# Performance work log

Hardware: AMD Instinct MI355X
Metric: run time of the kernel (lower is better)

The kernel has to match this reference:

```python
import jax, jax.numpy as jnp
import numpy as np

GRID_SIZE = 8
MARGIN = 1.0
NUM_NEG = 4
SOS_NEG = 8
LOSS_LAMBDA = 1.0
IMG_H, IMG_W = 960, 1280  # desc2 is the stride-GRID_SIZE feature map of this image
BIG = 5.0    # fill for radius-masked entries in FOS distance matrix (> max unit-desc dist 2)
HUGE = 1e6   # fill for invalid entries in SOS candidate scores


def _l2n(x, eps=1e-8):
    return x / (jnp.linalg.norm(x, axis=-1, keepdims=True) + eps)


def _pdist(a, b, eps=1e-12):
    # a: B x N x C, b: B x M x C -> B x N x M euclidean distances
    sq = (jnp.sum(a * a, -1)[..., :, None] + jnp.sum(b * b, -1)[..., None, :]
          - 2.0 * jnp.einsum('bnc,bmc->bnm', a, b))
    return jnp.sqrt(jnp.maximum(sq, eps))


def _bilinear(desc, pts):
    # desc: B x C x H x W, pts: B x N x 2 in (y, x) image-pixel coords -> B x N x C
    B, C, H, W = desc.shape
    g = pts / GRID_SIZE - 0.5  # image coords -> feature-grid coords
    gy = jnp.clip(g[..., 0], 0.0, H - 1.0)
    gx = jnp.clip(g[..., 1], 0.0, W - 1.0)
    y0 = jnp.clip(jnp.floor(gy).astype(jnp.int32), 0, H - 2)
    x0 = jnp.clip(jnp.floor(gx).astype(jnp.int32), 0, W - 2)
    wy = (gy - y0)[:, None, :]
    wx = (gx - x0)[:, None, :]
    flat = desc.reshape(B, C, H * W)
    gat = lambda yi, xi: jnp.take_along_axis(flat, (yi * W + xi)[:, None, :], axis=2)
    v00, v01 = gat(y0, x0), gat(y0, x0 + 1)
    v10, v11 = gat(y0 + 1, x0), gat(y0 + 1, x0 + 1)
    out = (v00 * (1 - wy) * (1 - wx) + v01 * (1 - wy) * wx
           + v10 * wy * (1 - wx) + v11 * wy * wx)
    return out.transpose(0, 2, 1)


def _forward(kp1, w_kp1, kp1_desc, desc2, homo12):
    r = 2.0 * GRID_SIZE  # spatial masking radius
    d1 = _l2n(kp1_desc)                       # B x N x C
    w_desc = _l2n(_bilinear(desc2, w_kp1))    # B x N x C interpolated warped descriptors

    # visibility of kp1 under homography homo12 (kp stored as (y, x))
    ones = jnp.ones_like(kp1[..., :1])
    p = jnp.concatenate([kp1[..., 1:2], kp1[..., 0:1], ones], -1)  # (x, y, 1)
    q = jnp.einsum('bij,bnj->bni', homo12, p)
    qx = q[..., 0] / (q[..., 2] + 1e-8)
    qy = q[..., 1] / (q[..., 2] + 1e-8)
    vis = ((qx >= 0) & (qx < IMG_W) & (qy >= 0) & (qy < IMG_H)).astype(d1.dtype)
    denom = jnp.sum(vis) + 1e-8

    # ---- FOS: hard quad triplet with radius masking ----
    pos = jnp.sqrt(jnp.sum((d1 - w_desc) ** 2, -1) + 1e-12)  # B x N
    D = _pdist(d1, w_desc)          # B x N x N cross descriptor distances
    s22 = _pdist(w_kp1, w_kp1)      # B x N x N warped-coordinate distances
    Dm = jnp.where(s22 <= r, BIG, D)  # mask spatial near-positives (incl. diagonal)
    neg1 = -jax.lax.top_k(-Dm, NUM_NEG)[0]                       # hardest negs per row anchor
    neg2 = -jax.lax.top_k(-Dm.transpose(0, 2, 1), NUM_NEG)[0]    # per column anchor
    t1 = jnp.mean(jax.nn.relu(MARGIN + pos[..., None] - neg1), -1)
    t2 = jnp.mean(jax.nn.relu(MARGIN + pos[..., None] - neg2), -1)
    fos = jnp.sum(vis * 0.5 * (t1 + t2)) / denom

    # ---- SOS: radius-masked second-order similarity regularizer ----
    s11 = _pdist(kp1, kp1)
    d11 = _pdist(d1, d1)
    d22 = _pdist(w_desc, w_desc)
    valid = (s11 > r) & (s22 > r)
    score = jnp.where(valid, d11, HUGE)
    nscore, idx = jax.lax.top_k(-score, SOS_NEG)  # sos_neg hardest valid neighbors
    sel_d11 = -nscore
    sel_d22 = jnp.take_along_axis(d22, idx, axis=2)
    diff2 = jnp.where(sel_d11 < HUGE * 0.1, (sel_d11 - sel_d22) ** 2, 0.0)
    sos_i = jnp.sqrt(jnp.sum(diff2, -1) + 1e-12)
    sos = jnp.sum(vis * sos_i) / denom

    return (fos + sos) * LOSS_LAMBDA


def setup_inputs() -> dict:
    key = jax.random.key(0)
    k1, k2, k3, k4, k5 = jax.random.split(key, 5)
    B, N, C, H, W = 2, 4096, 128, 120, 160
    scale = jnp.array([IMG_H - 1.0, IMG_W - 1.0], dtype=jnp.float32)
    kp1 = jax.random.uniform(k1, (B, N, 2), dtype=jnp.float32) * scale
    w_kp1 = jax.random.uniform(k2, (B, N, 2), dtype=jnp.float32) * scale
    kp1_desc = jax.random.normal(k3, (B, N, C), dtype=jnp.float32)
    desc2 = jax.random.normal(k4, (B, C, H, W), dtype=jnp.float32)
    homo12 = (jnp.tile(jnp.eye(3, dtype=jnp.float32), (B, 1, 1))
              + 0.001 * jax.random.normal(k5, (B, 3, 3), dtype=jnp.float32))
    return {'kp1': kp1, 'w_kp1': w_kp1, 'kp1_desc': kp1_desc,
            'desc2': desc2, 'homo12': homo12}


def reference(kp1, w_kp1, kp1_desc, desc2, homo12):
    return _forward(kp1, w_kp1, kp1_desc, desc2, homo12)
```

## Files before the change

kernel.cpp:

```cpp
#include <hip/hip_runtime.h>
#include <hip/hip_fp16.h>
#include <math.h>

#define NPTS 4096
#define CDIM 128
#define FH 120
#define FW 160
#define PIX (FH * FW)

typedef __attribute__((ext_vector_type(8))) short short8_t;
typedef __attribute__((ext_vector_type(4))) float float4_t;
typedef __attribute__((ext_vector_type(2))) unsigned short ushort2_t;

#define OFF_FRAG  0
#define OFF_WDB   1048576
#define OFF_JA    1572864
#define OFF_JB    1605632
#define OFF_POS   1622016
#define OFF_VIS   1630208
#define OFF_ACC   1638400
#define OFF_PARTS 1638416
#define OFF_D2T   2031632
#define OFF_END   4489232

__device__ __forceinline__ unsigned short f2bf(float f) {
  unsigned int u = __float_as_uint(f);
  u = (u + 0x7fffu + ((u >> 16) & 1u)) >> 16;
  return (unsigned short)u;
}

__device__ __forceinline__ float wavesum(float v) {
#pragma unroll
  for (int off = 1; off < 64; off <<= 1) v += __shfl_xor(v, off, 64);
  return v;
}

__global__ __launch_bounds__(256) void transpose_desc2(
    const float* __restrict__ d2, unsigned short* __restrict__ out) {
  __shared__ unsigned short tile[64][130];
  const int bp = blockIdx.x;
  const int b = bp / 300;
  const int p0 = (bp - b * 300) * 64;
  const int tid = threadIdx.x;
  const int grp = tid >> 6, lp = tid & 63;
#pragma unroll 4
  for (int r = 0; r < 32; ++r) {
    int c = (r << 2) | grp;
    float v = d2[((size_t)b * CDIM + c) * PIX + p0 + lp];
    tile[lp][c] = __half_as_ushort(__float2half(v));
  }
  __syncthreads();
  unsigned int* ob = (unsigned int*)(out + ((size_t)b * PIX + p0) * CDIM);
#pragma unroll
  for (int i = 0; i < 16; ++i) {
    int u = (i << 8) | tid;
    int p = u >> 6, cc = (u & 63) << 1;
    unsigned int lo = tile[p][cc], hi = tile[p][cc + 1];
    ob[u] = lo | (hi << 16);
  }
}

#define PREP_TAIL() do {                                                        \
  {                                                                             \
    const int T = (p & (NPTS - 1)) >> 4, cRow = p & 15;                         \
    const int kcL = lane >> 4, quadL = (lane >> 2) & 3, jjL = (lane & 3) * 2;   \
    const size_t off = (size_t)(quadL * 16 + cRow) * 8 + jjL;                   \
    const size_t tb = (((size_t)b * 256 + T) * 2) * 4;                          \
    ushort2_t st; st.x = f2bf(d0); st.y = f2bf(d1v);                            \
    ushort2_t sw; sw.x = f2bf(e0); sw.y = f2bf(e1);                             \
    *(ushort2_t*)(frag + (tb + kcL) * 512 + off) = st;                          \
    *(ushort2_t*)(frag + (tb + 4 + kcL) * 512 + off) = sw;                      \
    ushort2_t swr; swr.x = f2bf(e0); swr.y = f2bf(e1);                          \
    *(ushort2_t*)(wdb + (size_t)p * CDIM + c2) = swr;                           \
  }                                                                             \
  float dd0 = d0 - e0, dd1 = d1v - e1;                                          \
  float ssp = wavesum(dd0 * dd0 + dd1 * dd1);                                   \
  if (lane == 0) {                                                              \
    pos[p] = sqrtf(ssp + 1e-12f);                                               \
    float ky = kp1[p * 2 + 0], kx = kp1[p * 2 + 1];                             \
    jA[p] = make_float4(ky, kx, y, x);                                          \
    jB[p] = make_float2(n1, n2);                                                \
    const float* h = homo + b * 9;                                              \
    float t0 = h[0] * kx + h[1] * ky + h[2];                                    \
    float t1 = h[3] * kx + h[4] * ky + h[5];                                    \
    float t2 = h[6] * kx + h[7] * ky + h[8];                                    \
    float qx = t0 / (t2 + 1e-8f), qy = t1 / (t2 + 1e-8f);                       \
    vis[p] = (qx >= 0.0f && qx < 1280.0f && qy >= 0.0f && qy < 960.0f)          \
                 ? 1.0f : 0.0f;                                                 \
  }                                                                             \
} while (0)

__global__ __launch_bounds__(256) void prep_t(
    const float* __restrict__ kp1, const float* __restrict__ wkp1,
    const float* __restrict__ desc, const unsigned short* __restrict__ d2t,
    const float* __restrict__ homo,
    unsigned short* __restrict__ frag, unsigned short* __restrict__ wdb,
    float4* __restrict__ jA, float2* __restrict__ jB,
    float* __restrict__ pos, float* __restrict__ vis, float* __restrict__ acc) {
  const int tid = threadIdx.x;
  if (blockIdx.x == 0 && tid < 4) acc[tid] = 0.0f;
  const int p = blockIdx.x * 4 + (tid >> 6);
  const int lane = tid & 63;
  const int b = p >> 12;
  const int c2 = lane * 2;

  float2 v = *(const float2*)(desc + (size_t)p * CDIM + c2);
  float ss = wavesum(v.x * v.x + v.y * v.y);
  float inv = 1.0f / (sqrtf(ss) + 1e-8f);
  float d0 = v.x * inv, d1v = v.y * inv;
  float n1 = ss * inv * inv;

  float y = wkp1[p * 2 + 0], x = wkp1[p * 2 + 1];
  float gy = fminf(fmaxf(y * 0.125f - 0.5f, 0.0f), (float)(FH - 1));
  float gx = fminf(fmaxf(x * 0.125f - 0.5f, 0.0f), (float)(FW - 1));
  int y0 = (int)floorf(gy); y0 = min(max(y0, 0), FH - 2);
  int x0 = (int)floorf(gx); x0 = min(max(x0, 0), FW - 2);
  float wy = gy - (float)y0, wx = gx - (float)x0;
  float w00 = (1 - wy) * (1 - wx), w01 = (1 - wy) * wx;
  float w10 = wy * (1 - wx), w11 = wy * wx;
  const unsigned int* t00 = (const unsigned int*)
      (d2t + ((size_t)b * PIX + y0 * FW + x0) * CDIM) + lane;
  unsigned int u00 = t00[0], u01 = t00[64];
  unsigned int u10 = t00[FW * 64], u11 = t00[FW * 64 + 64];
  float2 f00 = __half22float2(*(const __half2*)&u00);
  float2 f01 = __half22float2(*(const __half2*)&u01);
  float2 f10 = __half22float2(*(const __half2*)&u10);
  float2 f11 = __half22float2(*(const __half2*)&u11);
  float wv0 = f00.x * w00 + f01.x * w01 + f10.x * w10 + f11.x * w11;
  float wv1 = f00.y * w00 + f01.y * w01 + f10.y * w10 + f11.y * w11;
  float ss2 = wavesum(wv0 * wv0 + wv1 * wv1);
  float inv2 = 1.0f / (sqrtf(ss2) + 1e-8f);
  float e0 = wv0 * inv2, e1 = wv1 * inv2;
  float n2 = ss2 * inv2 * inv2;

  PREP_TAIL();
}

__global__ __launch_bounds__(256) void prep_g(
    const float* __restrict__ kp1, const float* __restrict__ wkp1,
    const float* __restrict__ desc, const float* __restrict__ desc2,
    const float* __restrict__ homo,
    unsigned short* __restrict__ frag, unsigned short* __restrict__ wdb,
    float4* __restrict__ jA, float2* __restrict__ jB,
    float* __restrict__ pos, float* __restrict__ vis, float* __restrict__ acc) {
  const int tid = threadIdx.x;
  if (blockIdx.x == 0 && tid < 4) acc[tid] = 0.0f;
  const int p = blockIdx.x * 4 + (tid >> 6);
  const int lane = tid & 63;
  const int b = p >> 12;
  const int c2 = lane * 2;

  float2 v = *(const float2*)(desc + (size_t)p * CDIM + c2);
  float ss = wavesum(v.x * v.x + v.y * v.y);
  float inv = 1.0f / (sqrtf(ss) + 1e-8f);
  float d0 = v.x * inv, d1v = v.y * inv;
  float n1 = ss * inv * inv;

  float y = wkp1[p * 2 + 0], x = wkp1[p * 2 + 1];
  float gy = fminf(fmaxf(y * 0.125f - 0.5f, 0.0f), (float)(FH - 1));
  float gx = fminf(fmaxf(x * 0.125f - 0.5f, 0.0f), (float)(FW - 1));
  int y0 = (int)floorf(gy); y0 = min(max(y0, 0), FH - 2);
  int x0 = (int)floorf(gx); x0 = min(max(x0, 0), FW - 2);
  float wy = gy - (float)y0, wx = gx - (float)x0;
  float w00 = (1 - wy) * (1 - wx), w01 = (1 - wy) * wx;
  float w10 = wy * (1 - wx), w11 = wy * wx;
  const float* q0 = desc2 + ((size_t)b * CDIM + c2) * PIX + y0 * FW + x0;
  const float* q1 = q0 + PIX;
  float wv0 = q0[0] * w00 + q0[1] * w01 + q0[FW] * w10 + q0[FW + 1] * w11;
  float wv1 = q1[0] * w00 + q1[1] * w01 + q1[FW] * w10 + q1[FW + 1] * w11;
  float ss2 = wavesum(wv0 * wv0 + wv1 * wv1);
  float inv2 = 1.0f / (sqrtf(ss2) + 1e-8f);
  float e0 = wv0 * inv2, e1 = wv1 * inv2;
  float n2 = ss2 * inv2 * inv2;

  PREP_TAIL();
}

__device__ __forceinline__ void ins4m(float v, float* L) {
  float p0 = L[0]; L[0] = fmaxf(L[0], v);
  float p1 = L[1]; L[1] = __builtin_amdgcn_fmed3f(p0, L[1], v);
  float p2 = L[2]; L[2] = __builtin_amdgcn_fmed3f(p1, L[2], v);
  L[3] = __builtin_amdgcn_fmed3f(p2, L[3], v);
}
__device__ __forceinline__ void ins6m(float v, float* L) {
  float p0 = L[0]; L[0] = fmaxf(L[0], v);
  float p1 = L[1]; L[1] = __builtin_amdgcn_fmed3f(p0, L[1], v);
  float p2 = L[2]; L[2] = __builtin_amdgcn_fmed3f(p1, L[2], v);
  float p3 = L[3]; L[3] = __builtin_amdgcn_fmed3f(p2, L[3], v);
  float p4 = L[4]; L[4] = __builtin_amdgcn_fmed3f(p3, L[4], v);
  L[5] = __builtin_amdgcn_fmed3f(p4, L[5], v);
}
__device__ __forceinline__ void ins10m(float v, float* L) {
  float p0 = L[0]; L[0] = fmaxf(L[0], v);
  float pk = p0;
#pragma unroll
  for (int k = 1; k < 9; ++k) {
    float cur = L[k];
    L[k] = __builtin_amdgcn_fmed3f(pk, cur, v);
    pk = cur;
  }
  L[9] = __builtin_amdgcn_fmed3f(pk, L[9], v);
}

__device__ __forceinline__ float packkey(float s, int j) {
  return __uint_as_float((__float_as_uint(s) & 0xFFFFF000u) | (unsigned)j);
}

#define TILE_COMPUTE(AD, AW, NA, NB, J0) do {                                   \
  float4_t aD = {0,0,0,0}, aDt = {0,0,0,0}, a11 = {0,0,0,0};                    \
  _Pragma("unroll")                                                             \
  for (int kc = 0; kc < 4; ++kc) {                                              \
    aD  = __builtin_amdgcn_mfma_f32_16x16x32_bf16(AW[kc], Bd[kc], aD,  0,0,0);  \
    aDt = __builtin_amdgcn_mfma_f32_16x16x32_bf16(AD[kc], Bw[kc], aDt, 0,0,0);  \
    a11 = __builtin_amdgcn_mfma_f32_16x16x32_bf16(AD[kc], Bd[kc], a11, 0,0,0);  \
  }                                                                             \
  const float nj1[4] = {NA.x, NA.z, NB.x, NB.z};                                \
  const float nj2[4] = {NA.y, NA.w, NB.y, NB.w};                                \
  _Pragma("unroll")                                                             \
  for (int reg = 0; reg < 4; ++reg) {                                           \
    const int jj = (J0) + (quad << 2) + reg;                                    \
    ins4m(packkey(fmaf(2.0f, aD[reg],  -nj2[reg]), jj), fD);                    \
    ins4m(packkey(fmaf(2.0f, aDt[reg], -nj1[reg]), jj), fDt);                   \
    ins6m(packkey(fmaf(2.0f, a11[reg], -nj1[reg]), jj), fS);                    \
  }                                                                             \
} while (0)

__global__ __launch_bounds__(256, 3) void loss_main(
    const unsigned short* __restrict__ frag,
    const float2* __restrict__ jBg, float* __restrict__ parts) {
  __shared__ float mb[4][16][24];

  const int tid = threadIdx.x;
  const int bid = blockIdx.x;
  const int b = bid & 1;
  const int half = (bid >> 1) & 1;
  const int g = bid >> 2;
  const int i0 = g * 16;
  const int wave = tid >> 6, lane = tid & 63;
  const int c = lane & 15, quad = lane >> 4;
  const int base = b * NPTS;

  short8_t Bd[4], Bw[4];
  {
    const unsigned short* fb = frag + ((((size_t)b * 256 + g) * 2) * 4) * 512 + (size_t)lane * 8;
#pragma unroll
    for (int kc = 0; kc < 4; ++kc) {
      Bd[kc] = *(const short8_t*)(fb + kc * 512);
      Bw[kc] = *(const short8_t*)(fb + (4 + kc) * 512);
    }
  }

  float fD[4], fDt[4], fS[6];
#pragma unroll
  for (int k = 0; k < 4; ++k) { fD[k] = -1e30f; fDt[k] = -1e30f; }
#pragma unroll
  for (int k = 0; k < 6; ++k) fS[k] = -1e30f;

  const int jstart = (half << 11) | (wave << 9);
  const unsigned short* fa = frag + (((size_t)b * 256 + (jstart >> 4)) * 8) * 512 + (size_t)lane * 8;
  const float2* jbb = jBg + base;

  short8_t A0d[4], A0w[4], A1d[4], A1w[4];
#pragma unroll
  for (int kc = 0; kc < 4; ++kc) {
    A0d[kc] = *(const short8_t*)(fa + kc * 512);
    A0w[kc] = *(const short8_t*)(fa + (4 + kc) * 512);
  }
  float4 n0a = *(const float4*)(jbb + jstart + (quad << 2));
  float4 n0b = *(const float4*)(jbb + jstart + (quad << 2) + 2);
  float4 n1a, n1b;

  for (int t = 0; t < 32; t += 2) {
    const unsigned short* f1 = fa + 4096;
#pragma unroll
    for (int kc = 0; kc < 4; ++kc) {
      A1d[kc] = *(const short8_t*)(f1 + kc * 512);
      A1w[kc] = *(const short8_t*)(f1 + (4 + kc) * 512);
    }
    {
      const int j1 = jstart + ((t + 1) << 4);
      n1a = *(const float4*)(jbb + j1 + (quad << 2));
      n1b = *(const float4*)(jbb + j1 + (quad << 2) + 2);
    }
    TILE_COMPUTE(A0d, A0w, n0a, n0b, jstart + (t << 4));
    const unsigned short* f2 = fa + ((t + 2 < 32) ? 8192 : 0);
#pragma unroll
    for (int kc = 0; kc < 4; ++kc) {
      A0d[kc] = *(const short8_t*)(f2 + kc * 512);
      A0w[kc] = *(const short8_t*)(f2 + (4 + kc) * 512);
    }
    {
      const int j2 = jstart + (((t + 2) & 31) << 4);
      n0a = *(const float4*)(jbb + j2 + (quad << 2));
      n0b = *(const float4*)(jbb + j2 + (quad << 2) + 2);
    }
    TILE_COMPUTE(A1d, A1w, n1a, n1b, jstart + ((t + 1) << 4));
    fa += 8192;
  }

  float eD[6], eDt[6], eS[10];
#pragma unroll
  for (int k = 0; k < 4; ++k) { eD[k] = fD[k]; eDt[k] = fDt[k]; }
  eD[4] = eD[5] = eDt[4] = eDt[5] = -1e30f;
#pragma unroll
  for (int k = 0; k < 6; ++k) eS[k] = fS[k];
  eS[6] = eS[7] = eS[8] = eS[9] = -1e30f;

  {
    float tmp[10];
#pragma unroll
    for (int off = 16; off <= 32; off <<= 1) {
#pragma unroll
      for (int k = 0; k < 6; ++k) tmp[k] = eD[k];
#pragma unroll
      for (int k = 0; k < 6; ++k) ins6m(__shfl_xor(tmp[k], off, 64), eD);
#pragma unroll
      for (int k = 0; k < 6; ++k) tmp[k] = eDt[k];
#pragma unroll
      for (int k = 0; k < 6; ++k) ins6m(__shfl_xor(tmp[k], off, 64), eDt);
#pragma unroll
      for (int k = 0; k < 10; ++k) tmp[k] = eS[k];
#pragma unroll
      for (int k = 0; k < 10; ++k) ins10m(__shfl_xor(tmp[k], off, 64), eS);
    }
  }

#pragma unroll
  for (int h2 = 2; h2 >= 1; h2 >>= 1) {
    if (wave >= h2 && wave < 2 * h2 && lane < 16) {
      float* m = &mb[wave][lane][0];
#pragma unroll
      for (int k = 0; k < 6; ++k) { m[k] = eD[k]; m[6 + k] = eDt[k]; }
#pragma unroll
      for (int k = 0; k < 10; ++k) m[12 + k] = eS[k];
    }
    __syncthreads();
    if (wave < h2 && lane < 16) {
      const float* m = &mb[wave + h2][lane][0];
#pragma unroll
      for (int k = 0; k < 6; ++k) ins6m(m[k], eD);
#pragma unroll
      for (int k = 0; k < 6; ++k) ins6m(m[6 + k], eDt);
#pragma unroll
      for (int k = 0; k < 10; ++k) ins10m(m[12 + k], eS);
    }
  }

  if (wave == 0 && lane < 16) {
    float* P = parts + (size_t)(half * 24) * 8192 + (base + i0 + lane);
#pragma unroll
    for (int k = 0; k < 6; ++k) {
      P[(size_t)k * 8192] = eD[k];
      P[(size_t)(6 + k) * 8192] = eDt[k];
    }
#pragma unroll
    for (int k = 0; k < 10; ++k) P[(size_t)(12 + k) * 8192] = eS[k];
  }
}

__device__ __forceinline__ float bflo(unsigned int u) { return __uint_as_float(u << 16); }
__device__ __forceinline__ float bfhi(unsigned int u) { return __uint_as_float(u & 0xFFFF0000u); }

__global__ __launch_bounds__(256) void merge_filter(
    const float* __restrict__ parts, const float4* __restrict__ jAg,
    const float2* __restrict__ jBg, const float* __restrict__ posg,
    const float* __restrict__ visg, const unsigned short* __restrict__ wdb,
    float* __restrict__ accum, float* __restrict__ out) {
  __shared__ int sJ[256];
  __shared__ float sD11[256], sD22[256], sFos[32], sVis[32], sN2[32];
  const int tid = threadIdx.x;
  const int a0 = blockIdx.x * 32;

  if (tid < 32) {
    const int a = a0 + tid;
    const int base = a & ~(NPTS - 1);
    float fD[6], fDt[6], fS[10];
    const float* P = parts + a;
#pragma unroll
    for (int k = 0; k < 6; ++k) { fD[k] = P[(size_t)k * 8192]; fDt[k] = P[(size_t)(6 + k) * 8192]; }
#pragma unroll
    for (int k = 0; k < 10; ++k) fS[k] = P[(size_t)(12 + k) * 8192];
    {
      const float* Q = P + (size_t)24 * 8192;
#pragma unroll
      for (int k = 0; k < 6; ++k) {
        ins6m(Q[(size_t)k * 8192], fD);
        ins6m(Q[(size_t)(6 + k) * 8192], fDt);
      }
#pragma unroll
      for (int k = 0; k < 10; ++k) ins10m(Q[(size_t)(12 + k) * 8192], fS);
    }

    const float4 own = jAg[a];
    const float2 nb = jBg[a];
    const float pv = posg[a], vv = visg[a];
    float t1s = 0.0f, t2s = 0.0f;
    int got = 0;
#pragma unroll
    for (int k = 0; k < 6; ++k) {
      int j = (int)(__float_as_uint(fD[k]) & 0xFFFu);
      float4 jc = jAg[base + j];
      float dz = own.z - jc.z, dw = own.w - jc.w;
      if (got < 4 && dz * dz + dw * dw > 256.0f) {
        float d2 = nb.x - fD[k];
        t1s += fmaxf(1.0f + pv - sqrtf(fmaxf(d2, 1e-12f)), 0.0f);
        got++;
      }
    }
    got = 0;
#pragma unroll
    for (int k = 0; k < 6; ++k) {
      int j = (int)(__float_as_uint(fDt[k]) & 0xFFFu);
      float4 jc = jAg[base + j];
      float dz = own.z - jc.z, dw = own.w - jc.w;
      if (got < 4 && dz * dz + dw * dw > 256.0f) {
        float d2 = nb.y - fDt[k];
        t2s += fmaxf(1.0f + pv - sqrtf(fmaxf(d2, 1e-12f)), 0.0f);
        got++;
      }
    }
    int m = 0;
#pragma unroll
    for (int k = 0; k < 10; ++k) {
      int j = (int)(__float_as_uint(fS[k]) & 0xFFFu);
      float4 jc = jAg[base + j];
      float ay = own.x - jc.x, ax = own.y - jc.y;
      float wz = own.z - jc.z, ww = own.w - jc.w;
      if (m < 8 && ay * ay + ax * ax > 256.0f && wz * wz + ww * ww > 256.0f) {
        sJ[tid * 8 + m] = base + j;
        sD11[tid * 8 + m] = sqrtf(fmaxf(nb.x - fS[k], 1e-12f));
        m++;
      }
    }
    for (int k = m; k < 8; ++k) sJ[tid * 8 + k] = -1;
    sFos[tid] = vv * 0.125f * (t1s + t2s);
    sVis[tid] = vv;
    sN2[tid] = nb.y;
  }
  __syncthreads();

  {
    const int slot = tid;
    const int al = slot >> 3;
    const int j = sJ[slot];
    float d22 = 0.0f;
    if (j >= 0) {
      const uint4* pi = (const uint4*)(wdb + (size_t)(a0 + al) * CDIM);
      const uint4* pj = (const uint4*)(wdb + (size_t)j * CDIM);
      float dot = 0.0f;
#pragma unroll
      for (int qq = 0; qq < 16; ++qq) {
        uint4 ui = pi[qq], uj = pj[qq];
        dot = fmaf(bflo(ui.x), bflo(uj.x), dot); dot = fmaf(bfhi(ui.x), bfhi(uj.x), dot);
        dot = fmaf(bflo(ui.y), bflo(uj.y), dot); dot = fmaf(bfhi(ui.y), bfhi(uj.y), dot);
        dot = fmaf(bflo(ui.z), bflo(uj.z), dot); dot = fmaf(bfhi(ui.z), bfhi(uj.z), dot);
        dot = fmaf(bflo(ui.w), bflo(uj.w), dot); dot = fmaf(bfhi(ui.w), bfhi(uj.w), dot);
      }
      d22 = sqrtf(fmaxf(sN2[al] + jBg[j].y - 2.0f * dot, 1e-12f));
    }
    sD22[slot] = d22;
  }
  __syncthreads();

  float contrib = 0.0f, vsum = 0.0f;
  if (tid < 32) {
    float s = 0.0f;
#pragma unroll
    for (int k = 0; k < 8; ++k) {
      if (sJ[tid * 8 + k] >= 0) {
        float d = sD11[tid * 8 + k] - sD22[tid * 8 + k];
        s = fmaf(d, d, s);
      }
    }
    contrib = sFos[tid] + sVis[tid] * sqrtf(s + 1e-12f);
    vsum = sVis[tid];
  }
  if (tid < 64) {
#pragma unroll
    for (int off = 32; off >= 1; off >>= 1) {
      contrib += __shfl_down(contrib, off, 64);
      vsum += __shfl_down(vsum, off, 64);
    }
    if (tid == 0) {
      atomicAdd(&accum[0], contrib);
      atomicAdd(&accum[1], vsum);
      __threadfence();
      float old = atomicAdd(&accum[2], 1.0f);
      if (old == 255.0f) {
        float t = atomicAdd(&accum[0], 0.0f);
        float v = atomicAdd(&accum[1], 0.0f);
        out[0] = t / (v + 1e-8f);
      }
    }
  }
}

extern "C" void kernel_launch(void* const* d_in, const int* in_sizes, int n_in,
                              void* d_out, int out_size, void* d_ws, size_t ws_size,
                              hipStream_t stream) {
  (void)in_sizes; (void)n_in; (void)out_size;
  const float* kp1   = (const float*)d_in[0];
  const float* wkp1  = (const float*)d_in[1];
  const float* desc  = (const float*)d_in[2];
  const float* desc2 = (const float*)d_in[3];
  const float* homo  = (const float*)d_in[4];
  float* ws = (float*)d_ws;
  unsigned short* frag = (unsigned short*)(ws + OFF_FRAG);
  unsigned short* wdb  = (unsigned short*)(ws + OFF_WDB);
  float4* jA = (float4*)(ws + OFF_JA);
  float2* jB = (float2*)(ws + OFF_JB);
  float* pos = ws + OFF_POS;
  float* vis = ws + OFF_VIS;
  float* acc = ws + OFF_ACC;
  float* parts = ws + OFF_PARTS;
  unsigned short* d2t = (unsigned short*)(ws + OFF_D2T);

  if (ws_size >= (size_t)OFF_END * 4) {
    transpose_desc2<<<600, 256, 0, stream>>>(desc2, d2t);
    prep_t<<<2048, 256, 0, stream>>>(kp1, wkp1, desc, d2t, homo,
                                     frag, wdb, jA, jB, pos, vis, acc);
  } else {
    prep_g<<<2048, 256, 0, stream>>>(kp1, wkp1, desc, desc2, homo,
                                     frag, wdb, jA, jB, pos, vis, acc);
  }
  loss_main<<<1024, 256, 0, stream>>>(frag, jB, parts);
  merge_filter<<<256, 256, 0, stream>>>(parts, jA, jB, pos, vis, wdb, acc,
                                        (float*)d_out);
}
```

Before: 169.4 us.

## Stage shared j-tiles in LDS and split j range across eight segments

The main loss kernel now assigns each wave its own 16 query rows and has all four waves share a j-tile that is double-buffered in LDS through global_load_lds. Before, each wave streamed its own j-range from global memory into registers. The j dimension is split into eight segments instead of two, which removes the in-block LDS tree merge of top-k lists. The finalize kernel now merges eight partial lists and spreads the FOS and SOS selection across 96 threads instead of 32. Occupancy is raised to 4 blocks per SM. The cost is a __syncthreads per tile and four times as much partial-result traffic.

Measured after the change: 152.2 us. 10.2% less time.

```diff
diff --git a/kernel.cpp b/kernel.cpp
--- a/kernel.cpp
+++ b/kernel.cpp
@@ -19,8 +19,8 @@
 #define OFF_POS   1622016
 #define OFF_VIS   1630208
 #define OFF_ACC   1638400
-#define OFF_PARTS 1638416
 #define OFF_D2T   2031632
+#define OFF_PARTS 2031632
 #define OFF_END   4489232
 
 __device__ __forceinline__ unsigned short f2bf(float f) {
@@ -33,6 +33,12 @@
 #pragma unroll
   for (int off = 1; off < 64; off <<= 1) v += __shfl_xor(v, off, 64);
   return v;
+}
+
+typedef const __attribute__((address_space(1))) unsigned int gu32_t;
+typedef __attribute__((address_space(3))) unsigned int lu32_t;
+__device__ __forceinline__ void gl_lds16(const void* g, void* l) {
+  __builtin_amdgcn_global_load_lds((gu32_t*)g, (lu32_t*)l, 16, 0, 0);
 }
 
 __global__ __launch_bounds__(256) void transpose_desc2(
@@ -225,24 +231,26 @@
   }                                                                             \
 } while (0)
 
-__global__ __launch_bounds__(256, 3) void loss_main(
+__global__ __launch_bounds__(256, 4) void loss_main(
     const unsigned short* __restrict__ frag,
     const float2* __restrict__ jBg, float* __restrict__ parts) {
-  __shared__ float mb[4][16][24];
+  __shared__ __align__(16) unsigned short bufA[2][4096];
 
   const int tid = threadIdx.x;
   const int bid = blockIdx.x;
-  const int b = bid & 1;
-  const int half = (bid >> 1) & 1;
-  const int g = bid >> 2;
-  const int i0 = g * 16;
+  const int combo = ((bid & 7) << 1) | (bid >> 9);
+  const int b   = combo >> 3;
+  const int seg = combo & 7;
+  const int g   = (bid >> 3) & 63;
   const int wave = tid >> 6, lane = tid & 63;
-  const int c = lane & 15, quad = lane >> 4;
+  const int quad = lane >> 4;
   const int base = b * NPTS;
+  const int jbase = seg << 9;
 
   short8_t Bd[4], Bw[4];
   {
-    const unsigned short* fb = frag + ((((size_t)b * 256 + g) * 2) * 4) * 512 + (size_t)lane * 8;
+    const unsigned short* fb =
+        frag + (((size_t)b * 256 + (g * 4 + wave)) * 8) * 512 + (size_t)lane * 8;
 #pragma unroll
     for (int kc = 0; kc < 4; ++kc) {
       Bd[kc] = *(const short8_t*)(fb + kc * 512);
@@ -256,46 +264,35 @@
 #pragma unroll
   for (int k = 0; k < 6; ++k) fS[k] = -1e30f;
 
-  const int jstart = (half << 11) | (wave << 9);
-  const unsigned short* fa = frag + (((size_t)b * 256 + (jstart >> 4)) * 8) * 512 + (size_t)lane * 8;
+  const unsigned short* fa = frag + (((size_t)b * 256 + (jbase >> 4)) * 8) * 512;
   const float2* jbb = jBg + base;
-
-  short8_t A0d[4], A0w[4], A1d[4], A1w[4];
-#pragma unroll
-  for (int kc = 0; kc < 4; ++kc) {
-    A0d[kc] = *(const short8_t*)(fa + kc * 512);
-    A0w[kc] = *(const short8_t*)(fa + (4 + kc) * 512);
-  }
-  float4 n0a = *(const float4*)(jbb + jstart + (quad << 2));
-  float4 n0b = *(const float4*)(jbb + jstart + (quad << 2) + 2);
-  float4 n1a, n1b;
-
-  for (int t = 0; t < 32; t += 2) {
-    const unsigned short* f1 = fa + 4096;
+  const int ch = wave << 1;
+
+  gl_lds16(fa + (size_t)ch * 512 + lane * 8, &bufA[0][ch * 512]);
+  gl_lds16(fa + (size_t)(ch + 1) * 512 + lane * 8, &bufA[0][(ch + 1) * 512]);
+  __syncthreads();
+
+  int cur = 0;
+  for (int t = 0; t < 32; ++t) {
+    if (t + 1 < 32) {
+      const unsigned short* fn = fa + 4096;
+      gl_lds16(fn + (size_t)ch * 512 + lane * 8, &bufA[cur ^ 1][ch * 512]);
+      gl_lds16(fn + (size_t)(ch + 1) * 512 + lane * 8,
+               &bufA[cur ^ 1][(ch + 1) * 512]);
+    }
+    const int j0 = jbase + (t << 4);
+    float4 na = *(const float4*)(jbb + j0 + (quad << 2));
+    float4 nb = *(const float4*)(jbb + j0 + (quad << 2) + 2);
+    short8_t Ad[4], Aw[4];
 #pragma unroll
     for (int kc = 0; kc < 4; ++kc) {
-      A1d[kc] = *(const short8_t*)(f1 + kc * 512);
-      A1w[kc] = *(const short8_t*)(f1 + (4 + kc) * 512);
-    }
-    {
-      const int j1 = jstart + ((t + 1) << 4);
-      n1a = *(const float4*)(jbb + j1 + (quad << 2));
-      n1b = *(const float4*)(jbb + j1 + (quad << 2) + 2);
-    }
-    TILE_COMPUTE(A0d, A0w, n0a, n0b, jstart + (t << 4));
-    const unsigned short* f2 = fa + ((t + 2 < 32) ? 8192 : 0);
-#pragma unroll
-    for (int kc = 0; kc < 4; ++kc) {
-      A0d[kc] = *(const short8_t*)(f2 + kc * 512);
-      A0w[kc] = *(const short8_t*)(f2 + (4 + kc) * 512);
-    }
-    {
-      const int j2 = jstart + (((t + 2) & 31) << 4);
-      n0a = *(const float4*)(jbb + j2 + (quad << 2));
-      n0b = *(const float4*)(jbb + j2 + (quad << 2) + 2);
-    }
-    TILE_COMPUTE(A1d, A1w, n1a, n1b, jstart + ((t + 1) << 4));
-    fa += 8192;
+      Ad[kc] = *(const short8_t*)&bufA[cur][kc * 512 + (size_t)lane * 8];
+      Aw[kc] = *(const short8_t*)&bufA[cur][(4 + kc) * 512 + (size_t)lane * 8];
+    }
+    TILE_COMPUTE(Ad, Aw, na, nb, j0);
+    __syncthreads();
+    cur ^= 1;
+    fa += 4096;
   }
 
   float eD[6], eDt[6], eS[10];
@@ -325,29 +322,9 @@
     }
   }
 
-#pragma unroll
-  for (int h2 = 2; h2 >= 1; h2 >>= 1) {
-    if (wave >= h2 && wave < 2 * h2 && lane < 16) {
-      float* m = &mb[wave][lane][0];
-#pragma unroll
-      for (int k = 0; k < 6; ++k) { m[k] = eD[k]; m[6 + k] = eDt[k]; }
-#pragma unroll
-      for (int k = 0; k < 10; ++k) m[12 + k] = eS[k];
-    }
-    __syncthreads();
-    if (wave < h2 && lane < 16) {
-      const float* m = &mb[wave + h2][lane][0];
-#pragma unroll
-      for (int k = 0; k < 6; ++k) ins6m(m[k], eD);
-#pragma unroll
-      for (int k = 0; k < 6; ++k) ins6m(m[6 + k], eDt);
-#pragma unroll
-      for (int k = 0; k < 10; ++k) ins10m(m[12 + k], eS);
-    }
-  }
-
-  if (wave == 0 && lane < 16) {
-    float* P = parts + (size_t)(half * 24) * 8192 + (base + i0 + lane);
+  if (lane < 16) {
+    float* P = parts + (size_t)(seg * 22) * 8192 +
+               (base + g * 64 + wave * 16 + lane);
 #pragma unroll
     for (int k = 0; k < 6; ++k) {
       P[(size_t)k * 8192] = eD[k];
@@ -367,75 +344,73 @@
     const float* __restrict__ visg, const unsigned short* __restrict__ wdb,
     float* __restrict__ accum, float* __restrict__ out) {
   __shared__ int sJ[256];
-  __shared__ float sD11[256], sD22[256], sFos[32], sVis[32], sN2[32];
+  __shared__ float sD11[256], sD22[256], sT[64], sVis[32], sN2[32];
   const int tid = threadIdx.x;
   const int a0 = blockIdx.x * 32;
 
-  if (tid < 32) {
-    const int a = a0 + tid;
+  if (tid < 64) {
+    const int al = tid & 31;
+    const int type = tid >> 5;
+    const int a = a0 + al;
     const int base = a & ~(NPTS - 1);
-    float fD[6], fDt[6], fS[10];
-    const float* P = parts + a;
-#pragma unroll
-    for (int k = 0; k < 6; ++k) { fD[k] = P[(size_t)k * 8192]; fDt[k] = P[(size_t)(6 + k) * 8192]; }
-#pragma unroll
-    for (int k = 0; k < 10; ++k) fS[k] = P[(size_t)(12 + k) * 8192];
-    {
-      const float* Q = P + (size_t)24 * 8192;
-#pragma unroll
-      for (int k = 0; k < 6; ++k) {
-        ins6m(Q[(size_t)k * 8192], fD);
-        ins6m(Q[(size_t)(6 + k) * 8192], fDt);
-      }
-#pragma unroll
-      for (int k = 0; k < 10; ++k) ins10m(Q[(size_t)(12 + k) * 8192], fS);
-    }
-
+    float L[6];
+#pragma unroll
+    for (int k = 0; k < 6; ++k) L[k] = -1e30f;
+    const float* P = parts + (size_t)(type * 6) * 8192 + a;
+#pragma unroll
+    for (int s = 0; s < 8; ++s) {
+#pragma unroll
+      for (int k = 0; k < 6; ++k) ins6m(P[(size_t)(s * 22 + k) * 8192], L);
+    }
     const float4 own = jAg[a];
     const float2 nb = jBg[a];
-    const float pv = posg[a], vv = visg[a];
-    float t1s = 0.0f, t2s = 0.0f;
+    const float pv = posg[a];
+    const float nsel = type ? nb.y : nb.x;
+    float ts = 0.0f;
     int got = 0;
 #pragma unroll
     for (int k = 0; k < 6; ++k) {
-      int j = (int)(__float_as_uint(fD[k]) & 0xFFFu);
+      int j = (int)(__float_as_uint(L[k]) & 0xFFFu);
       float4 jc = jAg[base + j];
       float dz = own.z - jc.z, dw = own.w - jc.w;
       if (got < 4 && dz * dz + dw * dw > 256.0f) {
-        float d2 = nb.x - fD[k];
-        t1s += fmaxf(1.0f + pv - sqrtf(fmaxf(d2, 1e-12f)), 0.0f);
+        float d2 = nsel - L[k];
+        ts += fmaxf(1.0f + pv - sqrtf(fmaxf(d2, 1e-12f)), 0.0f);
         got++;
       }
     }
-    got = 0;
-#pragma unroll
-    for (int k = 0; k < 6; ++k) {
-      int j = (int)(__float_as_uint(fDt[k]) & 0xFFFu);
-      float4 jc = jAg[base + j];
-      float dz = own.z - jc.z, dw = own.w - jc.w;
-      if (got < 4 && dz * dz + dw * dw > 256.0f) {
-        float d2 = nb.y - fDt[k];
-        t2s += fmaxf(1.0f + pv - sqrtf(fmaxf(d2, 1e-12f)), 0.0f);
-        got++;
-      }
-    }
+    sT[tid] = ts;
+  } else if (tid < 96) {
+    const int al = tid - 64;
+    const int a = a0 + al;
+    const int base = a & ~(NPTS - 1);
+    float S[10];
+#pragma unroll
+    for (int k = 0; k < 10; ++k) S[k] = -1e30f;
+    const float* P = parts + (size_t)12 * 8192 + a;
+#pragma unroll
+    for (int s = 0; s < 8; ++s) {
+#pragma unroll
+      for (int k = 0; k < 10; ++k) ins10m(P[(size_t)(s * 22 + k) * 8192], S);
+    }
+    const float4 own = jAg[a];
+    const float2 nb = jBg[a];
     int m = 0;
 #pragma unroll
     for (int k = 0; k < 10; ++k) {
-      int j = (int)(__float_as_uint(fS[k]) & 0xFFFu);
+      int j = (int)(__float_as_uint(S[k]) & 0xFFFu);
       float4 jc = jAg[base + j];
       float ay = own.x - jc.x, ax = own.y - jc.y;
       float wz = own.z - jc.z, ww = own.w - jc.w;
       if (m < 8 && ay * ay + ax * ax > 256.0f && wz * wz + ww * ww > 256.0f) {
-        sJ[tid * 8 + m] = base + j;
-        sD11[tid * 8 + m] = sqrtf(fmaxf(nb.x - fS[k], 1e-12f));
+        sJ[al * 8 + m] = base + j;
+        sD11[al * 8 + m] = sqrtf(fmaxf(nb.x - S[k], 1e-12f));
         m++;
       }
     }
-    for (int k = m; k < 8; ++k) sJ[tid * 8 + k] = -1;
-    sFos[tid] = vv * 0.125f * (t1s + t2s);
-    sVis[tid] = vv;
-    sN2[tid] = nb.y;
+    for (int k = m; k < 8; ++k) sJ[al * 8 + k] = -1;
+    sVis[al] = visg[a];
+    sN2[al] = nb.y;
   }
   __syncthreads();
 
@@ -472,7 +447,7 @@
         s = fmaf(d, d, s);
       }
     }
-    contrib = sFos[tid] + sVis[tid] * sqrtf(s + 1e-12f);
+    contrib = sVis[tid] * (0.125f * (sT[tid] + sT[32 + tid]) + sqrtf(s + 1e-12f));
     vsum = sVis[tid];
   }
   if (tid < 64) {
```
